# Optimization experiments

Measured on AMD Instinct MI355X. Metric: run time of the kernel, lower is better.

The kernel has to match this reference:

```python
import jax, jax.numpy as jnp
import numpy as np
from jax import lax

B = 128
NODES = 304
T_STEPS = 20
HID = 64
GCN_IN = 20
N = B * NODES            # 38912 graph nodes
E = N * 16               # 622592 edges
BN_EPS = 1e-5


def setup_inputs() -> dict:
    key = jax.random.key(0)
    ks = jax.random.split(key, 32)
    rn = lambda k, s, sc=0.1: jax.random.normal(k, s, jnp.float32) * sc
    return {
        "data_x": jax.random.normal(ks[0], (N, GCN_IN), jnp.float32),
        "edge_index": jax.random.randint(ks[1], (2, E), 0, N),
        "edge_weight": jax.random.uniform(ks[2], (E,), jnp.float32),
        "tc1_w1": rn(ks[3], (HID, 1, 1, 3)), "tc1_b1": rn(ks[4], (HID,)),
        "tc1_w2": rn(ks[5], (HID, 1, 1, 3)), "tc1_b2": rn(ks[6], (HID,)),
        "tc1_w3": rn(ks[7], (HID, 1, 1, 3)), "tc1_b3": rn(ks[8], (HID,)),
        "gcn_W0": rn(ks[9], (GCN_IN, HID)), "gcn_b0": rn(ks[10], (HID,)),
        "bn0_g": jax.random.uniform(ks[11], (HID,), jnp.float32, 0.5, 1.5), "bn0_b": rn(ks[12], (HID,)),
        "gcn_W1": rn(ks[13], (HID, HID)), "gcn_b1": rn(ks[14], (HID,)),
        "bn1_g": jax.random.uniform(ks[15], (HID,), jnp.float32, 0.5, 1.5), "bn1_b": rn(ks[16], (HID,)),
        "tc2_w1": rn(ks[17], (1, HID, 1, 3)), "tc2_b1": rn(ks[18], (1,)),
        "tc2_w2": rn(ks[19], (1, HID, 1, 3)), "tc2_b2": rn(ks[20], (1,)),
        "tc2_w3": rn(ks[21], (1, HID, 1, 3)), "tc2_b3": rn(ks[22], (1,)),
        "bn2d_g": jax.random.uniform(ks[23], (NODES,), jnp.float32, 0.5, 1.5), "bn2d_b": rn(ks[24], (NODES,)),
        "fc_W": rn(ks[25], (21 * NODES, 2048), 0.01), "fc_b": rn(ks[26], (2048,)),
        "fc4_W": rn(ks[27], (2048, 300), 0.01), "fc4_b": rn(ks[28], (300,)),
    }


def _bn(x, g, b):
    # eval-mode BatchNorm with fresh running stats (mean=0, var=1)
    return x * (g / jnp.sqrt(1.0 + BN_EPS)) + b


def _temporal_conv(X, w1, b1, w2, b2, w3, b3):
    # X: [B, T, nodes, C] -> permute to NCHW [B, C, nodes, T]
    Xp = jnp.transpose(X, (0, 3, 2, 1))
    conv = lambda w, b: lax.conv_general_dilated(
        Xp, w, (1, 1), [(0, 0), (1, 1)],
        dimension_numbers=("NCHW", "OIHW", "NCHW")) + b[None, :, None, None]
    P = conv(w1, b1)
    Q = jax.nn.sigmoid(conv(w2, b2))
    H = jax.nn.relu(P * Q + conv(w3, b3))
    return jnp.transpose(H, (0, 3, 2, 1))  # back to [B, T, nodes, C_out]


def reference(data_x, edge_index, edge_weight,
              tc1_w1, tc1_b1, tc1_w2, tc1_b2, tc1_w3, tc1_b3,
              gcn_W0, gcn_b0, bn0_g, bn0_b,
              gcn_W1, gcn_b1, bn1_g, bn1_b,
              tc2_w1, tc2_b1, tc2_w2, tc2_b2, tc2_w3, tc2_b3,
              bn2d_g, bn2d_b, fc_W, fc_b, fc4_W, fc4_b):
    n = data_x.shape[0]
    b = n // NODES

    # ---- GCN norm (sym, self-loops w=1) ----
    row, col = edge_index[0], edge_index[1]
    loop = jnp.arange(n)
    rowF = jnp.concatenate([row, loop])
    colF = jnp.concatenate([col, loop])
    ewF = jnp.concatenate([edge_weight, jnp.ones((n,), data_x.dtype)])
    deg = jax.ops.segment_sum(ewF, colF, num_segments=n)
    dinv = lax.rsqrt(jnp.maximum(deg, 1e-12))
    norm = dinv[rowF] * ewF * dinv[colF]

    def gconv(x, W, bias):
        h = x @ W
        return jax.ops.segment_sum(h[rowF] * norm[:, None], colF, num_segments=n) + bias

    x = jax.nn.relu(_bn(gconv(data_x, gcn_W0, gcn_b0), bn0_g, bn0_b))
    x = jax.nn.relu(_bn(gconv(x, gcn_W1, gcn_b1), bn1_g, bn1_b))  # [N, HID]

    # ---- temporal conv 1 ----
    X = data_x.reshape(b, T_STEPS, NODES, 1)
    T0 = _temporal_conv(X, tc1_w1, tc1_b1, tc1_w2, tc1_b2, tc1_w3, tc1_b3)  # [B,20,304,HID]

    # gcn_feature.permute(1,0).reshape(-1, 1, nodes, HID)
    gfeat = x.T.reshape(b, 1, NODES, HID)

    T = jnp.concatenate([jax.nn.relu(T0), gfeat], axis=1)  # [B, 21, 304, HID]
    T = jax.nn.relu(T)

    # ---- temporal conv 2 ----
    T = _temporal_conv(T, tc2_w1, tc2_b1, tc2_w2, tc2_b2, tc2_w3, tc2_b3)  # [B,21,304,1]

    # BatchNorm2d over node channel (axis=2 here), eval-mode running stats
    T = T * (bn2d_g / jnp.sqrt(1.0 + BN_EPS))[None, None, :, None] + bn2d_b[None, None, :, None]

    T = T.reshape(b, -1)  # [B, 6384]
    T = jax.nn.relu(T @ fc_W + fc_b)
    return T @ fc4_W + fc4_b  # [B, 300]
```

## Files before the change

### kernel.cpp

```cpp
#include <hip/hip_runtime.h>

#define NODES   304
#define BATCH   128
#define TSTEPS  20
#define HID     64
#define GCNIN   20
#define NN      (BATCH*NODES)
#define NE      (NN*16)
#define SEGSZ   (NN/4)
#define BCAP    64
#define FC1_IN  (21*NODES)
#define KP1     6400
#define FC1_OUT 2048
#define FC2_OUT 300
#define NP2     304
#define BN_EPS  1e-5f

typedef __attribute__((ext_vector_type(8))) short short8;
typedef __attribute__((ext_vector_type(4))) float f32x4;
typedef __attribute__((ext_vector_type(2))) float f32x2;

static __device__ __forceinline__ short f2bf(float x) {
    unsigned u = __float_as_uint(x);
    unsigned r = (u + 0x7FFF + ((u >> 16) & 1)) >> 16;
    return (short)r;
}
static __device__ __forceinline__ float bf2f(unsigned short v) {
    return __uint_as_float((unsigned)v << 16);
}

static __device__ __forceinline__ float fast_sigmoid(float q) {
    return __builtin_amdgcn_rcpf(1.f + __expf(-q));
}

static __device__ __forceinline__ f32x2 pk_fma(f32x2 a, f32x2 b, f32x2 c) {
    f32x2 d;
    asm("v_pk_fma_f32 %0, %1, %2, %3" : "=v"(d) : "v"(a), "v"(b), "v"(c));
    return d;
}

template <int C>
static __device__ __forceinline__ float dppadd(float v) {
    return v + __int_as_float(
        __builtin_amdgcn_update_dpp(0, __float_as_int(v), C, 0xF, 0xF, false));
}
static __device__ __forceinline__ float rsum16(float v) {
    v = dppadd<0x128>(v);
    v = dppadd<0x124>(v);
    v = dppadd<0x122>(v);
    v = dppadd<0x121>(v);
    return v;
}

__global__ void k_bucket(const int* __restrict__ ei, const float* __restrict__ ew,
                         int* __restrict__ cnt, unsigned* __restrict__ bucket) {
    int e = blockIdx.x * blockDim.x + threadIdx.x;
    if (e < NE) {
        int c = ei[NE + e];
        int slot = atomicAdd(&cnt[c], 1);
        if (slot < BCAP) {
            unsigned v = ((unsigned)(unsigned short)f2bf(ew[e]) << 16) |
                         (unsigned)ei[e];
            bucket[((size_t)c << 6) + slot] = v;
        }
    }
}

__global__ __launch_bounds__(256) void k_cvtX(const float* __restrict__ X,
                                              const int* __restrict__ cnt,
                                              const unsigned* __restrict__ bucket,
                                              unsigned short* __restrict__ Xb,
                                              float* __restrict__ dinv) {
    int wv = threadIdx.x >> 5, f = threadIdx.x & 31;
    int n = blockIdx.x * 8 + wv;
    __shared__ float rs[8][2];

    unsigned e0 = bucket[((size_t)n << 6) + f];
    unsigned e1 = bucket[((size_t)n << 6) + 32 + f];
    int deg = cnt[n];
    float xv = (f < GCNIN) ? X[(size_t)n * GCNIN + f] : 0.f;

    int dcap = deg < BCAP ? deg : BCAP;
    float s = ((f < dcap) ? bf2f((unsigned short)(e0 >> 16)) : 0.f) +
              ((32 + f < dcap) ? bf2f((unsigned short)(e1 >> 16)) : 0.f);
    s = rsum16(s);
    if ((f & 15) == 0) rs[wv][f >> 4] = s;
    __syncthreads();

    float dv = rsqrtf(fmaxf(1.f + rs[wv][0] + rs[wv][1], 1e-12f));
    if (f == 0) dinv[n] = dv;
    Xb[(size_t)n * 32 + f] = (f < GCNIN) ? (unsigned short)f2bf(xv * dv)
                                         : (unsigned short)0;
}

static __device__ __forceinline__ void stage_partition(
    int deg, unsigned e, int f, int wv, int (*sIdx)[BCAP], float (*sWt)[BCAP],
    int& dcap) {
    dcap = deg < BCAP ? deg : BCAP;
    bool valid = f < dcap;
    int row = (int)(e & 0xffffu);
    float w = bf2f((unsigned short)(e >> 16));
    int q = (row >= SEGSZ) + (row >= 2 * SEGSZ) + (row >= 3 * SEGSZ);
    unsigned long long b0 = __ballot(valid && q == 0);
    unsigned long long b1 = __ballot(valid && q == 1);
    unsigned long long b2 = __ballot(valid && q == 2);
    unsigned long long b3 = __ballot(valid && q == 3);
    unsigned long long lmask = (1ULL << f) - 1;
    int pos = 0;
    if (q > 0) pos += __popcll(b0);
    if (q > 1) pos += __popcll(b1);
    if (q > 2) pos += __popcll(b2);
    unsigned long long mybal = (q == 0) ? b0 : (q == 1) ? b1 : (q == 2) ? b2 : b3;
    pos += __popcll(mybal & lmask);
    if (valid) {
        sIdx[wv][pos] = row;
        sWt[wv][pos] = w;
    }
}

__global__ __launch_bounds__(256) void k_gather20(const int* __restrict__ cnt,
                                                  const unsigned* __restrict__ bucket,
                                                  const float* __restrict__ dinv,
                                                  const unsigned short* __restrict__ Xb,
                                                  const float* __restrict__ W0,
                                                  const float* __restrict__ gb,
                                                  const float* __restrict__ bng,
                                                  const float* __restrict__ bnb,
                                                  const float* __restrict__ W1,
                                                  unsigned short* __restrict__ H1) {
    int wv = threadIdx.x >> 6, f = threadIdx.x & 63;
    int c = blockIdx.x * 4 + wv;
    int g = f >> 4, r = f & 15;
    __shared__ int sIdx[4][BCAP];
    __shared__ float sWt[4][BCAP];
    __shared__ float agg[4][32];
    __shared__ float xs[4][HID];

    unsigned be = bucket[((size_t)c << 6) + f];
    int deg = cnt[c];
    float dc = dinv[c];
    unsigned selfv = *(const unsigned*)(Xb + (size_t)c * 32 + 2 * r);

    int dcap;
    stage_partition(deg, be, f, wv, sIdx, sWt, dcap);
    __syncthreads();

    f32x2 acc2;
    acc2[0] = 0.f;
    acc2[1] = 0.f;
    for (int base = 0; base < dcap; base += 16) {
        int idx[4];
        float w[4];
#pragma unroll
        for (int i = 0; i < 4; i++) {
            int l = base + (i << 2) + g;
            int lc = (l < dcap) ? l : dcap - 1;
            idx[i] = sIdx[wv][lc];
            w[i] = (l < dcap) ? sWt[wv][lc] : 0.f;
        }
        unsigned vv[4];
#pragma unroll
        for (int i = 0; i < 4; i++)
            vv[i] = *(const unsigned*)(Xb + (size_t)idx[i] * 32 + 2 * r);
#pragma unroll
        for (int i = 0; i < 4; i++) {
            acc2[0] = fmaf(bf2f((unsigned short)(vv[i] & 0xffff)), w[i], acc2[0]);
            acc2[1] = fmaf(bf2f((unsigned short)(vv[i] >> 16)), w[i], acc2[1]);
        }
    }
    acc2[0] += __shfl_xor(acc2[0], 16);
    acc2[0] += __shfl_xor(acc2[0], 32);
    acc2[1] += __shfl_xor(acc2[1], 16);
    acc2[1] += __shfl_xor(acc2[1], 32);
    if (g == 0) {
        agg[wv][2 * r] = acc2[0] + bf2f((unsigned short)(selfv & 0xffff));
        agg[wv][2 * r + 1] = acc2[1] + bf2f((unsigned short)(selfv >> 16));
    }
    __syncthreads();

    float v = 0.f;
#pragma unroll
    for (int k = 0; k < GCNIN; k++) v = fmaf(agg[wv][k], W0[k * HID + f], v);
    float scale = bng[f] * rsqrtf(1.f + BN_EPS);
    float y = fmaxf(fmaf(v * dc + gb[f], scale, bnb[f]), 0.f);

    xs[wv][f] = y;
    __syncthreads();
    float h = 0.f;
#pragma unroll
    for (int k4 = 0; k4 < HID / 4; k4++) {
        float4 xv = *(const float4*)&xs[wv][k4 * 4];
        h = fmaf(xv.x, W1[(k4 * 4 + 0) * HID + f], h);
        h = fmaf(xv.y, W1[(k4 * 4 + 1) * HID + f], h);
        h = fmaf(xv.z, W1[(k4 * 4 + 2) * HID + f], h);
        h = fmaf(xv.w, W1[(k4 * 4 + 3) * HID + f], h);
    }
    H1[(size_t)c * HID + f] = (unsigned short)f2bf(h * dc);
}

__global__ __launch_bounds__(256) void k_gatherB(const int* __restrict__ cnt,
                                                 const unsigned* __restrict__ bucket,
                                                 const float* __restrict__ dinv,
                                                 const unsigned short* __restrict__ H,
                                                 const float* __restrict__ gb,
                                                 const float* __restrict__ bng,
                                                 const float* __restrict__ bnb,
                                                 float* __restrict__ XO) {
    int wv = threadIdx.x >> 6, f = threadIdx.x & 63;
    int c = blockIdx.x * 4 + wv;
    int g = f >> 4, r = f & 15;
    __shared__ int sIdx[4][BCAP];
    __shared__ float sWt[4][BCAP];

    unsigned be = bucket[((size_t)c << 6) + f];
    int deg = cnt[c];
    float dc = dinv[c];
    ushort4 selfv = *(const ushort4*)(H + (size_t)c * HID + 4 * r);

    int dcap;
    stage_partition(deg, be, f, wv, sIdx, sWt, dcap);
    __syncthreads();

    float a0 = 0.f, a1 = 0.f, a2 = 0.f, a3 = 0.f;
    for (int base = 0; base < dcap; base += 16) {
        int idx[4];
        float w[4];
#pragma unroll
        for (int i = 0; i < 4; i++) {
            int l = base + (i << 2) + g;
            int lc = (l < dcap) ? l : dcap - 1;
            idx[i] = sIdx[wv][lc];
            w[i] = (l < dcap) ? sWt[wv][lc] : 0.f;
        }
        ushort4 hv[4];
#pragma unroll
        for (int i = 0; i < 4; i++)
            hv[i] = *(const ushort4*)(H + (size_t)idx[i] * HID + 4 * r);
#pragma unroll
        for (int i = 0; i < 4; i++) {
            a0 = fmaf(bf2f(hv[i].x), w[i], a0);
            a1 = fmaf(bf2f(hv[i].y), w[i], a1);
            a2 = fmaf(bf2f(hv[i].z), w[i], a2);
            a3 = fmaf(bf2f(hv[i].w), w[i], a3);
        }
    }
    a0 += __shfl_xor(a0, 16); a0 += __shfl_xor(a0, 32);
    a1 += __shfl_xor(a1, 16); a1 += __shfl_xor(a1, 32);
    a2 += __shfl_xor(a2, 16); a2 += __shfl_xor(a2, 32);
    a3 += __shfl_xor(a3, 16); a3 += __shfl_xor(a3, 32);

    if (g == 0) {
        float4 scv = *(const float4*)&bng[4 * r];
        float4 bbv = *(const float4*)&bnb[4 * r];
        float4 gbv = *(const float4*)&gb[4 * r];
        float rr = rsqrtf(1.f + BN_EPS);
        float4 o;
        o.x = fmaxf(fmaf((a0 + bf2f(selfv.x)) * dc + gbv.x, scv.x * rr, bbv.x), 0.f);
        o.y = fmaxf(fmaf((a1 + bf2f(selfv.y)) * dc + gbv.y, scv.y * rr, bbv.y), 0.f);
        o.z = fmaxf(fmaf((a2 + bf2f(selfv.z)) * dc + gbv.z, scv.z * rr, bbv.z), 0.f);
        o.w = fmaxf(fmaf((a3 + bf2f(selfv.w)) * dc + gbv.w, scv.w * rr, bbv.w), 0.f);
        *(float4*)(XO + (size_t)c * HID + 4 * r) = o;
    }
}

__global__ __launch_bounds__(256) void k_xpose(const float* __restrict__ x2,
                                               float* __restrict__ x2t) {
    __shared__ float tile[64][65];
    int n0 = blockIdx.x * 64;
    for (int i = threadIdx.x; i < 4096; i += 256) {
        int r = i >> 6, h = i & 63;
        tile[r][h] = x2[(size_t)(n0 + r) * 64 + h];
    }
    __syncthreads();
    for (int i = threadIdx.x; i < 4096; i += 256) {
        int h = i >> 6, c = i & 63;
        x2t[(size_t)h * NN + n0 + c] = tile[c][h];
    }
}

static __device__ __forceinline__ void load12(const float* base, f32x2 P[2][3]) {
    float4 f0 = *(const float4*)(base);
    float4 f1 = *(const float4*)(base + 4);
    float4 f2 = *(const float4*)(base + 8);
    P[0][0][0] = f0.x; P[0][0][1] = f0.w;
    P[0][1][0] = f0.y; P[0][1][1] = f1.x;
    P[0][2][0] = f0.z; P[0][2][1] = f1.y;
    P[1][0][0] = f1.z; P[1][0][1] = f2.y;
    P[1][1][0] = f1.w; P[1][1][1] = f2.z;
    P[1][2][0] = f2.x; P[1][2][1] = f2.w;
}

__global__ __launch_bounds__(256) void k_temporal2(
    const float* __restrict__ data_x, const float* __restrict__ x2t,
    const float* __restrict__ w1, const float* __restrict__ b1,
    const float* __restrict__ w2, const float* __restrict__ b2,
    const float* __restrict__ w3, const float* __restrict__ b3,
    const float* __restrict__ v1, const float* __restrict__ vb1,
    const float* __restrict__ v2, const float* __restrict__ vb2,
    const float* __restrict__ v3, const float* __restrict__ vb3,
    const float* __restrict__ bn2g, const float* __restrict__ bn2b,
    short* __restrict__ Ab) {
    int bn0 = blockIdx.x * 16;
    int b = bn0 / NODES, node0 = bn0 % NODES;
    int tid = threadIdx.x;
    int p = tid >> 4;
    int c0 = (tid & 15) << 2;
    int node = node0 + p;

    __shared__ float xs[16][22];
    __shared__ float wlds[1344];

    if (tid < 192) {
        wlds[tid] = w1[tid];
        wlds[192 + tid] = w2[tid];
        wlds[384 + tid] = w3[tid];
        wlds[576 + tid] = v1[tid];
        wlds[768 + tid] = v2[tid];
        wlds[960 + tid] = v3[tid];
    }
    if (tid < 64) {
        wlds[1152 + tid] = b1[tid];
        wlds[1216 + tid] = b2[tid];
        wlds[1280 + tid] = b3[tid];
    }
    for (int i = tid; i < 320; i += 256) {
        int t = i >> 4, pp = i & 15;
        xs[pp][t + 1] = data_x[b * (TSTEPS * NODES) + t * NODES + node0 + pp];
    }
    if (tid < 16) { xs[tid][0] = 0.f; xs[tid][21] = 0.f; }

    float cb1 = vb1[0], cb2 = vb2[0], cb3 = vb3[0];
    float s2 = bn2g[node] * rsqrtf(1.f + BN_EPS);
    float bb2 = bn2b[node];
    short* dst = Ab + (size_t)b * KP1;

    __syncthreads();

    f32x2 A1p[2][3], A2p[2][3], A3p[2][3], B1p[2], B2p[2], B3p[2];
    f32x2 U1p[2][3], U2p[2][3], U3p[2][3];
    load12(&wlds[0 + c0 * 3], A1p);
    load12(&wlds[192 + c0 * 3], A2p);
    load12(&wlds[384 + c0 * 3], A3p);
    load12(&wlds[576 + c0 * 3], U1p);
    load12(&wlds[768 + c0 * 3], U2p);
    load12(&wlds[960 + c0 * 3], U3p);
    {
        float4 t1 = *(const float4*)&wlds[1152 + c0];
        float4 t2 = *(const float4*)&wlds[1216 + c0];
        float4 t3 = *(const float4*)&wlds[1280 + c0];
        B1p[0][0] = t1.x; B1p[0][1] = t1.y; B1p[1][0] = t1.z; B1p[1][1] = t1.w;
        B2p[0][0] = t2.x; B2p[0][1] = t2.y; B2p[1][0] = t2.z; B2p[1][1] = t2.w;
        B3p[0][0] = t3.x; B3p[0][1] = t3.y; B3p[1][0] = t3.z; B3p[1][1] = t3.w;
    }

    f32x2 hA2[2] = {}, hB2[2] = {}, hC2[2];
    float xr0 = xs[p][0], xr1 = xs[p][1];

#pragma unroll
    for (int j = 0; j <= 21; j++) {
        if (j < 20) {
            float xr2 = xs[p][j + 2];
            f32x2 x0d, x1d, x2d;
            x0d[0] = xr0; x0d[1] = xr0;
            x1d[0] = xr1; x1d[1] = xr1;
            x2d[0] = xr2; x2d[1] = xr2;
#pragma unroll
            for (int cp = 0; cp < 2; cp++) {
                f32x2 pv = pk_fma(A1p[cp][2], x2d,
                            pk_fma(A1p[cp][1], x1d, pk_fma(A1p[cp][0], x0d, B1p[cp])));
                f32x2 qv = pk_fma(A2p[cp][2], x2d,
                            pk_fma(A2p[cp][1], x1d, pk_fma(A2p[cp][0], x0d, B2p[cp])));
                f32x2 rv = pk_fma(A3p[cp][2], x2d,
                            pk_fma(A3p[cp][1], x1d, pk_fma(A3p[cp][0], x0d, B3p[cp])));
                hC2[cp][0] = fmaxf(fmaf(pv[0], fast_sigmoid(qv[0]), rv[0]), 0.f);
                hC2[cp][1] = fmaxf(fmaf(pv[1], fast_sigmoid(qv[1]), rv[1]), 0.f);
            }
            xr0 = xr1;
            xr1 = xr2;
        } else if (j == 20) {
            const float4 gv = *(const float4*)(x2t + (size_t)(b >> 1) * NN +
                                               (b & 1) * (NODES * HID) + node * HID + c0);
            hC2[0][0] = fmaxf(gv.x, 0.f);
            hC2[0][1] = fmaxf(gv.y, 0.f);
            hC2[1][0] = fmaxf(gv.z, 0.f);
            hC2[1][1] = fmaxf(gv.w, 0.f);
        } else {
            hC2[0][0] = 0.f; hC2[0][1] = 0.f;
            hC2[1][0] = 0.f; hC2[1][1] = 0.f;
        }
        if (j >= 1) {
            int w = j - 1;
            f32x2 pa, qa, ra;
            pa[0] = 0.f; pa[1] = 0.f;
            qa[0] = 0.f; qa[1] = 0.f;
            ra[0] = 0.f; ra[1] = 0.f;
#pragma unroll
            for (int cp = 0; cp < 2; cp++) {
                pa = pk_fma(U1p[cp][0], hA2[cp], pa);
                pa = pk_fma(U1p[cp][1], hB2[cp], pa);
                pa = pk_fma(U1p[cp][2], hC2[cp], pa);
                qa = pk_fma(U2p[cp][0], hA2[cp], qa);
                qa = pk_fma(U2p[cp][1], hB2[cp], qa);
                qa = pk_fma(U2p[cp][2], hC2[cp], qa);
                ra = pk_fma(U3p[cp][0], hA2[cp], ra);
                ra = pk_fma(U3p[cp][1], hB2[cp], ra);
                ra = pk_fma(U3p[cp][2], hC2[cp], ra);
            }
            float pp_ = rsum16(pa[0] + pa[1]);
            float qq_ = rsum16(qa[0] + qa[1]);
            float rr_ = rsum16(ra[0] + ra[1]);
            float P = pp_ + cb1, Q = qq_ + cb2, R = rr_ + cb3;
            float hv = fmaxf(fmaf(P, fast_sigmoid(Q), R), 0.f);
            if ((tid & 15) == 0) dst[w * NODES + node] = f2bf(fmaf(hv, s2, bb2));
        }
        hA2[0] = hB2[0]; hA2[1] = hB2[1];
        hB2[0] = hC2[0]; hB2[1] = hC2[1];
    }
}

#define KSPL1 8
#define KCH1  (KP1 / KSPL1)
__global__ __launch_bounds__(256) void k_gemm1f(const short* __restrict__ Ab,
                                                const float* __restrict__ fcW,
                                                float* __restrict__ part) {
    int lane = threadIdx.x & 63, wv = threadIdx.x >> 6;
    int r = lane & 15, kg = lane >> 4;
    int nb = blockIdx.x * 64, sp = blockIdx.y;

    f32x4 acc[2][4] = {};
    const short* a0 = Ab + (size_t)(wv * 32 + r) * KP1;
    const short* a1 = a0 + (size_t)16 * KP1;

    int k0 = sp * KCH1 + kg * 8;
    const float* wp = fcW + (size_t)k0 * FC1_OUT + nb + r;
    bool tailblk = (sp == KSPL1 - 1);

#pragma unroll 1
    for (int s = 0; s < KCH1 / 32; s++, k0 += 32) {
        short8 av0 = *(const short8*)(a0 + k0);
        short8 av1 = *(const short8*)(a1 + k0);
        short8 bv[4];
        if (tailblk && s == KCH1 / 32 - 1) {
#pragma unroll
            for (int f = 0; f < 4; f++)
#pragma unroll
                for (int i = 0; i < 8; i++) {
                    float v = (k0 + i < FC1_IN) ? wp[(size_t)i * FC1_OUT + f * 16] : 0.f;
                    bv[f][i] = f2bf(v);
                }
        } else {
#pragma unroll
            for (int f = 0; f < 4; f++)
#pragma unroll
                for (int i = 0; i < 8; i++)
                    bv[f][i] = f2bf(wp[(size_t)i * FC1_OUT + f * 16]);
        }
        acc[0][0] = __builtin_amdgcn_mfma_f32_16x16x32_bf16(av0, bv[0], acc[0][0], 0, 0, 0);
        acc[1][0] = __builtin_amdgcn_mfma_f32_16x16x32_bf16(av1, bv[0], acc[1][0], 0, 0, 0);
        acc[0][1] = __builtin_amdgcn_mfma_f32_16x16x32_bf16(av0, bv[1], acc[0][1], 0, 0, 0);
        acc[1][1] = __builtin_amdgcn_mfma_f32_16x16x32_bf16(av1, bv[1], acc[1][1], 0, 0, 0);
        acc[0][2] = __builtin_amdgcn_mfma_f32_16x16x32_bf16(av0, bv[2], acc[0][2], 0, 0, 0);
        acc[1][2] = __builtin_amdgcn_mfma_f32_16x16x32_bf16(av1, bv[2], acc[1][2], 0, 0, 0);
        acc[0][3] = __builtin_amdgcn_mfma_f32_16x16x32_bf16(av0, bv[3], acc[0][3], 0, 0, 0);
        acc[1][3] = __builtin_amdgcn_mfma_f32_16x16x32_bf16(av1, bv[3], acc[1][3], 0, 0, 0);
        wp += (size_t)32 * FC1_OUT;
    }

    float* dst = part + (size_t)sp * BATCH * FC1_OUT;
#pragma unroll
    for (int m = 0; m < 2; m++)
#pragma unroll
        for (int f = 0; f < 4; f++)
#pragma unroll
            for (int j = 0; j < 4; j++) {
                int row = wv * 32 + m * 16 + kg * 4 + j;
                int col = nb + f * 16 + r;
                dst[(size_t)row * FC1_OUT + col] = acc[m][f][j];
            }
}

__global__ __launch_bounds__(256) void k_reduce1(const float* __restrict__ part,
                                                 const float* __restrict__ bias,
                                                 short* __restrict__ Ab2) {
    int idx = blockIdx.x * 256 + threadIdx.x;
    int o = idx & (FC1_OUT - 1);
    float s = bias[o];
#pragma unroll
    for (int sp = 0; sp < KSPL1; sp++) s += part[(size_t)sp * BATCH * FC1_OUT + idx];
    Ab2[idx] = f2bf(fmaxf(s, 0.f));
}

#define KSPL2 8
#define KCH2  (FC1_OUT / KSPL2)
__global__ __launch_bounds__(256) void k_gemm2f(const short* __restrict__ Ab,
                                                const float* __restrict__ fc4W,
                                                float* __restrict__ part) {
    int lane = threadIdx.x & 63, wv = threadIdx.x >> 6;
    int r = lane & 15, kg = lane >> 4;
    int nb = blockIdx.x * 16, sp = blockIdx.y;

    f32x4 acc[2] = {};
    const short* a0 = Ab + (size_t)(wv * 32 + r) * FC1_OUT;
    const short* a1 = a0 + (size_t)16 * FC1_OUT;
    int col = nb + r;
    int colc = (col < FC2_OUT) ? col : FC2_OUT - 1;

    int k0 = sp * KCH2 + kg * 8;
    const float* wp = fc4W + (size_t)k0 * FC2_OUT + colc;
#pragma unroll 1
    for (int s = 0; s < KCH2 / 32; s++, k0 += 32) {
        short8 av0 = *(const short8*)(a0 + k0);
        short8 av1 = *(const short8*)(a1 + k0);
        short8 bv;
#pragma unroll
        for (int i = 0; i < 8; i++) bv[i] = f2bf(wp[(size_t)i * FC2_OUT]);
        acc[0] = __builtin_amdgcn_mfma_f32_16x16x32_bf16(av0, bv, acc[0], 0, 0, 0);
        acc[1] = __builtin_amdgcn_mfma_f32_16x16x32_bf16(av1, bv, acc[1], 0, 0, 0);
        wp += (size_t)32 * FC2_OUT;
    }

    float* dst = part + (size_t)sp * BATCH * NP2;
#pragma unroll
    for (int m = 0; m < 2; m++)
#pragma unroll
        for (int j = 0; j < 4; j++) {
            int row = wv * 32 + m * 16 + kg * 4 + j;
            dst[(size_t)row * NP2 + col] = acc[m][j];
        }
}

__global__ __launch_bounds__(256) void k_reduce2(const float* __restrict__ part,
                                                 const float* __restrict__ bias,
                                                 float* __restrict__ out) {
    int idx = blockIdx.x * 256 + threadIdx.x;
    if (idx >= BATCH * NP2) return;
    int b = idx / NP2, o = idx % NP2;
    float s = 0.f;
#pragma unroll
    for (int sp = 0; sp < KSPL2; sp++) s += part[(size_t)sp * BATCH * NP2 + idx];
    if (o < FC2_OUT) out[(size_t)b * FC2_OUT + o] = s + bias[o];
}

extern "C" void kernel_launch(void* const* d_in, const int* in_sizes, int n_in,
                              void* d_out, int out_size, void* d_ws, size_t ws_size,
                              hipStream_t stream) {
    const float* data_x = (const float*)d_in[0];
    const int* ei = (const int*)d_in[1];
    const float* ew = (const float*)d_in[2];
    const float* tc1w1 = (const float*)d_in[3];
    const float* tc1b1 = (const float*)d_in[4];
    const float* tc1w2 = (const float*)d_in[5];
    const float* tc1b2 = (const float*)d_in[6];
    const float* tc1w3 = (const float*)d_in[7];
    const float* tc1b3 = (const float*)d_in[8];
    const float* W0 = (const float*)d_in[9];
    const float* gb0 = (const float*)d_in[10];
    const float* bn0g = (const float*)d_in[11];
    const float* bn0b = (const float*)d_in[12];
    const float* W1 = (const float*)d_in[13];
    const float* gb1 = (const float*)d_in[14];
    const float* bn1g = (const float*)d_in[15];
    const float* bn1b = (const float*)d_in[16];
    const float* tc2w1 = (const float*)d_in[17];
    const float* tc2b1 = (const float*)d_in[18];
    const float* tc2w2 = (const float*)d_in[19];
    const float* tc2b2 = (const float*)d_in[20];
    const float* tc2w3 = (const float*)d_in[21];
    const float* tc2b3 = (const float*)d_in[22];
    const float* bn2g = (const float*)d_in[23];
    const float* bn2b = (const float*)d_in[24];
    const float* fcW = (const float*)d_in[25];
    const float* fcb = (const float*)d_in[26];
    const float* fc4W = (const float*)d_in[27];
    const float* fc4b = (const float*)d_in[28];
    float* out = (float*)d_out;

    char* ws = (char*)d_ws;
    float* x2 = (float*)(ws + 0);
    short* Ab = (short*)(ws + 9961472);
    const size_t ARENA = 9961472 + 1638400;

    size_t off = ARENA;
    auto alloc = [&](size_t bytes) -> void* {
        void* p = ws + off;
        off = (off + bytes + 255) & ~(size_t)255;
        return p;
    };
    unsigned* bucket = (unsigned*)alloc((size_t)NN * BCAP * 4);
    int* cnt = (int*)alloc((size_t)NN * 4);
    float* dinv = (float*)alloc((size_t)NN * 4);
    unsigned short* Xb = (unsigned short*)alloc((size_t)NN * 32 * 2);
    unsigned short* h1 = (unsigned short*)alloc((size_t)NN * HID * 2);

    float* x2t = (float*)(ws + ARENA);

    off = ARENA;
    float* part1 = (float*)alloc((size_t)KSPL1 * BATCH * FC1_OUT * 4);
    short* Ab2 = (short*)alloc((size_t)BATCH * FC1_OUT * 2);
    float* part2 = (float*)alloc((size_t)KSPL2 * BATCH * NP2 * 4);
    (void)ws_size; (void)in_sizes; (void)n_in; (void)out_size;

    hipMemsetAsync(cnt, 0, (size_t)NN * 4, stream);
    k_bucket<<<(NE + 255) / 256, 256, 0, stream>>>(ei, ew, cnt, bucket);

    k_cvtX<<<NN / 8, 256, 0, stream>>>(data_x, cnt, bucket, Xb, dinv);
    k_gather20<<<NN / 4, 256, 0, stream>>>(cnt, bucket, dinv, Xb, W0, gb0, bn0g,
                                           bn0b, W1, h1);
    k_gatherB<<<NN / 4, 256, 0, stream>>>(cnt, bucket, dinv, h1, gb1, bn1g, bn1b, x2);

    k_xpose<<<NN / 64, 256, 0, stream>>>(x2, x2t);

    hipMemsetAsync(Ab, 0, (size_t)BATCH * KP1 * 2, stream);
    k_temporal2<<<NN / 16, 256, 0, stream>>>(data_x, x2t, tc1w1, tc1b1, tc1w2, tc1b2,
                                             tc1w3, tc1b3, tc2w1, tc2b1, tc2w2, tc2b2,
                                             tc2w3, tc2b3, bn2g, bn2b, Ab);

    {
        dim3 g(FC1_OUT / 64, KSPL1);
        k_gemm1f<<<g, 256, 0, stream>>>(Ab, fcW, part1);
    }
    k_reduce1<<<BATCH * FC1_OUT / 256, 256, 0, stream>>>(part1, fcb, Ab2);
    {
        dim3 g(NP2 / 16, KSPL2);
        k_gemm2f<<<g, 256, 0, stream>>>(Ab2, fc4W, part2);
    }
    k_reduce2<<<(BATCH * NP2 + 255) / 256, 256, 0, stream>>>(part2, fc4b, out);
}
```

Measured before the change: 184.9 us.

## Drop transpose kernel by gathering GCN features directly; use packed bf16 conversion

Removes the separate k_xpose launch. k_temporal2 now reads the GCN output x2 with strided scalar loads, issued early in the kernel so their latency overlaps the weight staging. Separately, weight conversion in both FC GEMMs uses the hardware v_cvt_pk_bf16_f32 instruction in place of manual rounding. This cuts one kernel launch plus an intermediate write and read, and reduces ALU work in the GEMM inner loops. The cost is uncoalesced strided gathers in the temporal kernel.

```diff
diff --git a/kernel.cpp b/kernel.cpp
--- a/kernel.cpp
+++ b/kernel.cpp
@@ -19,6 +19,7 @@
 typedef __attribute__((ext_vector_type(8))) short short8;
 typedef __attribute__((ext_vector_type(4))) float f32x4;
 typedef __attribute__((ext_vector_type(2))) float f32x2;
+typedef __attribute__((ext_vector_type(4))) int i32x4;
 
 static __device__ __forceinline__ short f2bf(float x) {
     unsigned u = __float_as_uint(x);
@@ -27,6 +28,12 @@
 }
 static __device__ __forceinline__ float bf2f(unsigned short v) {
     return __uint_as_float((unsigned)v << 16);
+}
+
+static __device__ __forceinline__ int cvtpk(float a, float b) {
+    int r;
+    asm("v_cvt_pk_bf16_f32 %0, %1, %2" : "=v"(r) : "v"(a), "v"(b));
+    return r;
 }
 
 static __device__ __forceinline__ float fast_sigmoid(float q) {
@@ -263,21 +270,6 @@
     }
 }
 
-__global__ __launch_bounds__(256) void k_xpose(const float* __restrict__ x2,
-                                               float* __restrict__ x2t) {
-    __shared__ float tile[64][65];
-    int n0 = blockIdx.x * 64;
-    for (int i = threadIdx.x; i < 4096; i += 256) {
-        int r = i >> 6, h = i & 63;
-        tile[r][h] = x2[(size_t)(n0 + r) * 64 + h];
-    }
-    __syncthreads();
-    for (int i = threadIdx.x; i < 4096; i += 256) {
-        int h = i >> 6, c = i & 63;
-        x2t[(size_t)h * NN + n0 + c] = tile[c][h];
-    }
-}
-
 static __device__ __forceinline__ void load12(const float* base, f32x2 P[2][3]) {
     float4 f0 = *(const float4*)(base);
     float4 f1 = *(const float4*)(base + 4);
@@ -291,7 +283,7 @@
 }
 
 __global__ __launch_bounds__(256) void k_temporal2(
-    const float* __restrict__ data_x, const float* __restrict__ x2t,
+    const float* __restrict__ data_x, const float* __restrict__ x2,
     const float* __restrict__ w1, const float* __restrict__ b1,
     const float* __restrict__ w2, const float* __restrict__ b2,
     const float* __restrict__ w3, const float* __restrict__ b3,
@@ -309,6 +301,13 @@
 
     __shared__ float xs[16][22];
     __shared__ float wlds[1344];
+
+    int n2b = (b & 1) * (NODES * HID) + node * HID + c0;
+    int jcol = b >> 1;
+    float g0 = x2[(size_t)(n2b + 0) * HID + jcol];
+    float g1 = x2[(size_t)(n2b + 1) * HID + jcol];
+    float g2 = x2[(size_t)(n2b + 2) * HID + jcol];
+    float g3 = x2[(size_t)(n2b + 3) * HID + jcol];
 
     if (tid < 192) {
         wlds[tid] = w1[tid];
@@ -378,12 +377,10 @@
             xr0 = xr1;
             xr1 = xr2;
         } else if (j == 20) {
-            const float4 gv = *(const float4*)(x2t + (size_t)(b >> 1) * NN +
-                                               (b & 1) * (NODES * HID) + node * HID + c0);
-            hC2[0][0] = fmaxf(gv.x, 0.f);
-            hC2[0][1] = fmaxf(gv.y, 0.f);
-            hC2[1][0] = fmaxf(gv.z, 0.f);
-            hC2[1][1] = fmaxf(gv.w, 0.f);
+            hC2[0][0] = fmaxf(g0, 0.f);
+            hC2[0][1] = fmaxf(g1, 0.f);
+            hC2[1][0] = fmaxf(g2, 0.f);
+            hC2[1][1] = fmaxf(g3, 0.f);
         } else {
             hC2[0][0] = 0.f; hC2[0][1] = 0.f;
             hC2[1][0] = 0.f; hC2[1][1] = 0.f;
@@ -442,18 +439,32 @@
         short8 bv[4];
         if (tailblk && s == KCH1 / 32 - 1) {
 #pragma unroll
-            for (int f = 0; f < 4; f++)
-#pragma unroll
-                for (int i = 0; i < 8; i++) {
-                    float v = (k0 + i < FC1_IN) ? wp[(size_t)i * FC1_OUT + f * 16] : 0.f;
-                    bv[f][i] = f2bf(v);
-                }
+            for (int f = 0; f < 4; f++) {
+                float wf[8];
+#pragma unroll
+                for (int i = 0; i < 8; i++)
+                    wf[i] = (k0 + i < FC1_IN) ? wp[(size_t)i * FC1_OUT + f * 16] : 0.f;
+                i32x4 pk;
+                pk[0] = cvtpk(wf[0], wf[1]);
+                pk[1] = cvtpk(wf[2], wf[3]);
+                pk[2] = cvtpk(wf[4], wf[5]);
+                pk[3] = cvtpk(wf[6], wf[7]);
+                bv[f] = __builtin_bit_cast(short8, pk);
+            }
         } else {
 #pragma unroll
-            for (int f = 0; f < 4; f++)
+            for (int f = 0; f < 4; f++) {
+                float wf[8];
 #pragma unroll
                 for (int i = 0; i < 8; i++)
-                    bv[f][i] = f2bf(wp[(size_t)i * FC1_OUT + f * 16]);
+                    wf[i] = wp[(size_t)i * FC1_OUT + f * 16];
+                i32x4 pk;
+                pk[0] = cvtpk(wf[0], wf[1]);
+                pk[1] = cvtpk(wf[2], wf[3]);
+                pk[2] = cvtpk(wf[4], wf[5]);
+                pk[3] = cvtpk(wf[6], wf[7]);
+                bv[f] = __builtin_bit_cast(short8, pk);
+            }
         }
         acc[0][0] = __builtin_amdgcn_mfma_f32_16x16x32_bf16(av0, bv[0], acc[0][0], 0, 0, 0);
         acc[1][0] = __builtin_amdgcn_mfma_f32_16x16x32_bf16(av1, bv[0], acc[1][0], 0, 0, 0);
@@ -511,9 +522,15 @@
     for (int s = 0; s < KCH2 / 32; s++, k0 += 32) {
         short8 av0 = *(const short8*)(a0 + k0);
         short8 av1 = *(const short8*)(a1 + k0);
-        short8 bv;
-#pragma unroll
-        for (int i = 0; i < 8; i++) bv[i] = f2bf(wp[(size_t)i * FC2_OUT]);
+        float wf[8];
+#pragma unroll
+        for (int i = 0; i < 8; i++) wf[i] = wp[(size_t)i * FC2_OUT];
+        i32x4 pk;
+        pk[0] = cvtpk(wf[0], wf[1]);
+        pk[1] = cvtpk(wf[2], wf[3]);
+        pk[2] = cvtpk(wf[4], wf[5]);
+        pk[3] = cvtpk(wf[6], wf[7]);
+        short8 bv = __builtin_bit_cast(short8, pk);
         acc[0] = __builtin_amdgcn_mfma_f32_16x16x32_bf16(av0, bv, acc[0], 0, 0, 0);
         acc[1] = __builtin_amdgcn_mfma_f32_16x16x32_bf16(av1, bv, acc[1], 0, 0, 0);
         wp += (size_t)32 * FC2_OUT;
@@ -592,8 +609,6 @@
     unsigned short* Xb = (unsigned short*)alloc((size_t)NN * 32 * 2);
     unsigned short* h1 = (unsigned short*)alloc((size_t)NN * HID * 2);
 
-    float* x2t = (float*)(ws + ARENA);
-
     off = ARENA;
     float* part1 = (float*)alloc((size_t)KSPL1 * BATCH * FC1_OUT * 4);
     short* Ab2 = (short*)alloc((size_t)BATCH * FC1_OUT * 2);
@@ -608,10 +623,8 @@
                                            bn0b, W1, h1);
     k_gatherB<<<NN / 4, 256, 0, stream>>>(cnt, bucket, dinv, h1, gb1, bn1g, bn1b, x2);
 
-    k_xpose<<<NN / 64, 256, 0, stream>>>(x2, x2t);
-
     hipMemsetAsync(Ab, 0, (size_t)BATCH * KP1 * 2, stream);
-    k_temporal2<<<NN / 16, 256, 0, stream>>>(data_x, x2t, tc1w1, tc1b1, tc1w2, tc1b2,
+    k_temporal2<<<NN / 16, 256, 0, stream>>>(data_x, x2, tc1w1, tc1b1, tc1w2, tc1b2,
                                              tc1w3, tc1b3, tc2w1, tc2b1, tc2w2, tc2b2,
                                              tc2w3, tc2b3, bn2g, bn2b, Ab);
 
```

Result: faster. 179.7 us (-2.8%).
